# Kernel optimization log

Measured on AMD Instinct MI355X. Metric: run time of the kernel, lower is better.

Reference implementation:

```python
import jax, jax.numpy as jnp
import numpy as np

D_MODEL = 1024
N_HEADS = 16
B, T = 2, 2048


def setup_inputs() -> dict:
    key = jax.random.key(0)
    kx, kqkv, ko = jax.random.split(key, 3)
    x = jax.random.normal(kx, (B, T, D_MODEL), dtype=jnp.float32)
    # flax Linear default init (lecun_normal ~ scaled); plain scaled normal is fine for a baseline
    Wqkv = jax.random.normal(kqkv, (D_MODEL, 3 * D_MODEL), dtype=jnp.float32) / np.sqrt(D_MODEL)
    Wo = jax.random.normal(ko, (D_MODEL, D_MODEL), dtype=jnp.float32) / np.sqrt(D_MODEL)
    return {"x": x, "Wqkv": Wqkv, "Wo": Wo}


def reference(x, Wqkv, Wo):
    Bx, Tx, C = x.shape
    H = N_HEADS
    Hd = C // H
    scale = C ** (-0.5)  # NOTE: module scales by d_model**-0.5, not head_dim**-0.5
    qkv = x @ Wqkv  # [B, T, 3C]
    q, k, v = jnp.split(qkv, 3, axis=-1)
    q = q.reshape(Bx, Tx, H, Hd).transpose(0, 2, 1, 3)  # [B,H,T,Hd]
    k = k.reshape(Bx, Tx, H, Hd).transpose(0, 2, 1, 3)
    v = v.reshape(Bx, Tx, H, Hd).transpose(0, 2, 1, 3)
    attn = jnp.einsum('bhid,bhjd->bhij', q, k) * scale  # [B,H,T,T]
    mask = jnp.tril(jnp.ones((Tx, Tx), dtype=jnp.bool_))
    attn = jnp.where(mask[None, None], attn, jnp.finfo(attn.dtype).min)
    attn = jax.nn.softmax(attn.astype(jnp.float32), axis=-1).astype(attn.dtype)
    out = jnp.einsum('bhij,bhjd->bhid', attn, v)  # [B,H,T,Hd]
    out = out.transpose(0, 2, 1, 3).reshape(Bx, Tx, C)
    return out @ Wo
```

## Files before the change

### kernel.cpp

```cpp
#include <hip/hip_runtime.h>
#include <cstdint>
#include <math.h>

#define D_MODEL 1024
#define N_HEADS 16
#define HEAD_DIM 64
#define BB 2
#define TT 2048
#define QSCALE 0.04508422002778011f
#define MSTATIC 12.0f

typedef float f32x4 __attribute__((ext_vector_type(4)));
typedef __bf16 bf16x8 __attribute__((ext_vector_type(8)));

__device__ inline ushort f2bf(float f) {
    union { float f; uint32_t u; } c; c.f = f;
    uint32_t u = c.u;
    uint32_t r = (u + 0x7FFFu + ((u >> 16) & 1u)) >> 16;
    return (ushort)r;
}
__device__ inline ushort f2bf_hw(float f) {
    __bf16 h = (__bf16)f;
    return __builtin_bit_cast(ushort, h);
}

__device__ inline void load_lds16(const ushort* g, ushort* lds_uniform_base) {
    __builtin_amdgcn_global_load_lds(
        (const __attribute__((address_space(1))) uint32_t*)g,
        (__attribute__((address_space(3))) uint32_t*)lds_uniform_base, 16, 0, 0);
}

__global__ __launch_bounds__(256) void conv_x(
    const float4* __restrict__ in, ushort4* __restrict__ out, int n4)
{
    int i = blockIdx.x * 256 + threadIdx.x;
    if (i < n4) {
        float4 v = in[i];
        ushort4 u;
        u.x = f2bf(v.x); u.y = f2bf(v.y); u.z = f2bf(v.z); u.w = f2bf(v.w);
        out[i] = u;
    }
}

__global__ __launch_bounds__(256) void transpose_f32_bf16(
    const float* __restrict__ in, ushort* __restrict__ out, int R, int C)
{
    __shared__ ushort tile[32][33];
    int tx = threadIdx.x;
    int ty = threadIdx.y;
    int c0 = blockIdx.x * 32;
    int r0 = blockIdx.y * 32;
#pragma unroll
    for (int i = 0; i < 32; i += 8)
        tile[ty + i][tx] = f2bf(in[(size_t)(r0 + ty + i) * C + (c0 + tx)]);
    __syncthreads();
#pragma unroll
    for (int i = 0; i < 32; i += 8)
        out[(size_t)(c0 + ty + i) * R + (r0 + tx)] = tile[tx][ty + i];
}

__global__ __launch_bounds__(256) void transpose_v_bf16(
    const ushort* __restrict__ in, ushort* __restrict__ out)
{
    int z = blockIdx.z;
    const ushort* ip = in + (size_t)z * TT * HEAD_DIM;
    ushort* op = out + (size_t)z * TT * HEAD_DIM;
    __shared__ ushort tile[32][33];
    int tx = threadIdx.x, ty = threadIdx.y;
    int d0 = blockIdx.x * 32;
    int t0 = blockIdx.y * 32;
#pragma unroll
    for (int i = 0; i < 32; i += 8)
        tile[ty + i][tx] = ip[(size_t)(t0 + ty + i) * HEAD_DIM + d0 + tx];
    __syncthreads();
#pragma unroll
    for (int i = 0; i < 32; i += 8)
        op[(size_t)(d0 + ty + i) * TT + t0 + tx] = tile[tx][ty + i];
}

__device__ inline void gemm128_mainloop(
    const ushort* __restrict__ A, const ushort* __restrict__ BT,
    int rowBase, int colBase, ushort* Al, ushort* Bl,
    f32x4 acc[4][4], int wave, int lane)
{
    const int K = D_MODEL;
    int lr = lane & 15, quad = lane >> 4;
    int lrow = lane >> 2;
    int kq = lane & 3;
    int mq = (wave >> 1) * 64, nq = (wave & 1) * 64;

    const ushort* gA0 = A + (size_t)(rowBase + wave * 32 + lrow) * K + kq * 8;
    const ushort* gA1 = gA0 + (size_t)16 * K;
    const ushort* gB0 = BT + (size_t)(colBase + wave * 32 + lrow) * K + kq * 8;
    const ushort* gB1 = gB0 + (size_t)16 * K;
    ushort* lA0 = Al + (wave * 32) * 32;
    ushort* lA1 = Al + (wave * 32 + 16) * 32;
    ushort* lB0 = Bl + (wave * 32) * 32;
    ushort* lB1 = Bl + (wave * 32 + 16) * 32;

    for (int kt = 0; kt < K / 32; ++kt) {
        __syncthreads();
        int ko = kt * 32;
        load_lds16(gA0 + ko, lA0);
        load_lds16(gA1 + ko, lA1);
        load_lds16(gB0 + ko, lB0);
        load_lds16(gB1 + ko, lB1);
        __syncthreads();
        bf16x8 af[4], bf[4];
#pragma unroll
        for (int mi = 0; mi < 4; ++mi)
            af[mi] = *(const bf16x8*)(Al + (mq + mi * 16 + lr) * 32 + quad * 8);
#pragma unroll
        for (int ni = 0; ni < 4; ++ni)
            bf[ni] = *(const bf16x8*)(Bl + (nq + ni * 16 + lr) * 32 + quad * 8);
#pragma unroll
        for (int mi = 0; mi < 4; ++mi)
#pragma unroll
            for (int ni = 0; ni < 4; ++ni)
                acc[mi][ni] = __builtin_amdgcn_mfma_f32_16x16x32_bf16(
                    af[mi], bf[ni], acc[mi][ni], 0, 0, 0);
    }
}

__global__ __launch_bounds__(256) void gemm_qkv(
    const ushort* __restrict__ A, const ushort* __restrict__ BT,
    ushort* __restrict__ Qo, ushort* __restrict__ Ko, ushort* __restrict__ Vo)
{
    __shared__ ushort Al[128 * 32];
    __shared__ ushort Bl[128 * 32];
    int tid = threadIdx.x;
    int wave = tid >> 6, lane = tid & 63;
    int lr = lane & 15, quad = lane >> 4;
    int rowBase = blockIdx.y * 128;
    int colBase = blockIdx.x * 128;
    f32x4 acc[4][4] = {};
    gemm128_mainloop(A, BT, rowBase, colBase, Al, Bl, acc, wave, lane);

    int mq = (wave >> 1) * 64, nq = (wave & 1) * 64;
#pragma unroll
    for (int ni = 0; ni < 4; ++ni) {
        int n = colBase + nq + ni * 16 + lr;
        int s = n >> 10;
        int cc = n & 1023;
        int h = cc >> 6, d = cc & 63;
        ushort* dst = (s == 0) ? Qo : (s == 1 ? Ko : Vo);
        float scale = (s == 0) ? QSCALE : 1.0f;
#pragma unroll
        for (int mi = 0; mi < 4; ++mi) {
#pragma unroll
            for (int i = 0; i < 4; ++i) {
                int m = rowBase + mq + mi * 16 + quad * 4 + i;
                int b = m >> 11, t = m & 2047;
                int bh = b * N_HEADS + h;
                dst[((size_t)bh * TT + t) * HEAD_DIM + d] = f2bf(acc[mi][ni][i] * scale);
            }
        }
    }
}

__global__ __launch_bounds__(256) void gemm_plain(
    const ushort* __restrict__ A, const ushort* __restrict__ BT,
    float* __restrict__ O, int N)
{
    const int K = D_MODEL;
    __shared__ ushort Al[128 * 32];
    __shared__ ushort Bl[64 * 32];
    int tid = threadIdx.x;
    int wave = tid >> 6, lane = tid & 63;
    int lr = lane & 15, quad = lane >> 4;
    int lrow = lane >> 2, kq = lane & 3;
    int rowBase = blockIdx.y * 128;
    int colBase = blockIdx.x * 64;
    int mq = (wave >> 1) * 64, nq = (wave & 1) * 32;

    const ushort* gA0 = A + (size_t)(rowBase + wave * 32 + lrow) * K + kq * 8;
    const ushort* gA1 = gA0 + (size_t)16 * K;
    const ushort* gB0 = BT + (size_t)(colBase + wave * 32 + lrow) * K + kq * 8;
    const ushort* gB1 = gB0 + (size_t)16 * K;
    ushort* lA0 = Al + (wave * 32) * 32;
    ushort* lA1 = Al + (wave * 32 + 16) * 32;
    ushort* lB0 = Bl + (wave * 32) * 32;
    ushort* lB1 = Bl + (wave * 32 + 16) * 32;

    f32x4 acc[4][2] = {};
    for (int kt = 0; kt < K / 32; ++kt) {
        __syncthreads();
        int ko = kt * 32;
        load_lds16(gA0 + ko, lA0);
        load_lds16(gA1 + ko, lA1);
        if (wave < 2) {
            load_lds16(gB0 + ko, lB0);
            load_lds16(gB1 + ko, lB1);
        }
        __syncthreads();
        bf16x8 af[4], bf[2];
#pragma unroll
        for (int mi = 0; mi < 4; ++mi)
            af[mi] = *(const bf16x8*)(Al + (mq + mi * 16 + lr) * 32 + quad * 8);
#pragma unroll
        for (int ni = 0; ni < 2; ++ni)
            bf[ni] = *(const bf16x8*)(Bl + (nq + ni * 16 + lr) * 32 + quad * 8);
#pragma unroll
        for (int mi = 0; mi < 4; ++mi)
#pragma unroll
            for (int ni = 0; ni < 2; ++ni)
                acc[mi][ni] = __builtin_amdgcn_mfma_f32_16x16x32_bf16(
                    af[mi], bf[ni], acc[mi][ni], 0, 0, 0);
    }

#pragma unroll
    for (int mi = 0; mi < 4; ++mi)
#pragma unroll
        for (int ni = 0; ni < 2; ++ni) {
            int n = colBase + nq + ni * 16 + lr;
#pragma unroll
            for (int i = 0; i < 4; ++i) {
                int m = rowBase + mq + mi * 16 + quad * 4 + i;
                O[(size_t)m * N + n] = acc[mi][ni][i];
            }
        }
}

__global__ __launch_bounds__(512) void attn_flash(
    const ushort* __restrict__ Q,
    const ushort* __restrict__ K,
    const ushort* __restrict__ VT,
    ushort* __restrict__ AO)
{
    int bid = blockIdx.x;
    int bh  = bid & 31;
    int idx = bid >> 5;
    int qi  = (idx < 8) ? idx : (23 - idx);
    int tid = threadIdx.x;
    int wave = tid >> 6;
    int pair = wave & 3;
    int half = wave >> 2;
    int lane = tid & 63;
    int quad = lane >> 4, lr = lane & 15;
    int qw = qi * 128 + pair * 32;

    const ushort* Qb = Q  + (size_t)bh * TT * HEAD_DIM;
    const ushort* Kb = K  + (size_t)bh * TT * HEAD_DIM;
    const ushort* Vb = VT + (size_t)bh * HEAD_DIM * TT;

    __shared__ ushort pbuf[8][32][40];
    __shared__ float comb[4][10][64][4];
    ushort (*P)[40] = pbuf[wave];

    bf16x8 qa[2][2];
#pragma unroll
    for (int r = 0; r < 2; ++r)
#pragma unroll
        for (int s = 0; s < 2; ++s)
            qa[r][s] = *(const bf16x8*)(Qb + (size_t)(qw + r * 16 + lr) * HEAD_DIM
                                           + s * 32 + quad * 8);

    f32x4 o[2][4] = {};
    f32x4 l[2] = {};

    bf16x8 ones;
#pragma unroll
    for (int j = 0; j < 8; ++j) ones[j] = (__bf16)1.0f;

    int ktiles = (qw >> 5) + 1;
    bf16x8 kbp[2][2], vbp[4];
    if (half < ktiles) {
        int k0 = half << 5;
#pragma unroll
        for (int c = 0; c < 2; ++c)
#pragma unroll
            for (int s = 0; s < 2; ++s)
                kbp[c][s] = *(const bf16x8*)(Kb + (size_t)(k0 + c * 16 + lr) * HEAD_DIM
                                                + s * 32 + quad * 8);
#pragma unroll
        for (int d = 0; d < 4; ++d)
            vbp[d] = *(const bf16x8*)(Vb + (size_t)(d * 16 + lr) * TT + k0 + quad * 8);
    }

    for (int kt = half; kt < ktiles; kt += 2) {
        bf16x8 kb[2][2], vb[4];
#pragma unroll
        for (int c = 0; c < 2; ++c)
#pragma unroll
            for (int s = 0; s < 2; ++s) kb[c][s] = kbp[c][s];
#pragma unroll
        for (int d = 0; d < 4; ++d) vb[d] = vbp[d];

        int kn = kt + 2;
        if (kn < ktiles) {
            int k0n = kn << 5;
#pragma unroll
            for (int c = 0; c < 2; ++c)
#pragma unroll
                for (int s = 0; s < 2; ++s)
                    kbp[c][s] = *(const bf16x8*)(Kb + (size_t)(k0n + c * 16 + lr) * HEAD_DIM
                                                    + s * 32 + quad * 8);
#pragma unroll
            for (int d = 0; d < 4; ++d)
                vbp[d] = *(const bf16x8*)(Vb + (size_t)(d * 16 + lr) * TT + k0n + quad * 8);
        }

        f32x4 sc[2][2];
#pragma unroll
        for (int r = 0; r < 2; ++r)
#pragma unroll
            for (int c = 0; c < 2; ++c)
#pragma unroll
                for (int i = 0; i < 4; ++i) sc[r][c][i] = -MSTATIC;
#pragma unroll
        for (int r = 0; r < 2; ++r)
#pragma unroll
            for (int c = 0; c < 2; ++c) {
                sc[r][c] = __builtin_amdgcn_mfma_f32_16x16x32_bf16(qa[r][0], kb[c][0], sc[r][c], 0, 0, 0);
                sc[r][c] = __builtin_amdgcn_mfma_f32_16x16x32_bf16(qa[r][1], kb[c][1], sc[r][c], 0, 0, 0);
            }
        if (kt == ktiles - 1) {
#pragma unroll
            for (int r = 0; r < 2; ++r)
#pragma unroll
                for (int c = 0; c < 2; ++c)
#pragma unroll
                    for (int i = 0; i < 4; ++i)
                        if (c * 16 + lr > r * 16 + quad * 4 + i) sc[r][c][i] = -3e38f;
        }

#pragma unroll
        for (int r = 0; r < 2; ++r)
#pragma unroll
            for (int c = 0; c < 2; ++c)
#pragma unroll
                for (int i = 0; i < 4; ++i)
                    P[r * 16 + quad * 4 + i][c * 16 + lr] =
                        f2bf_hw(__builtin_amdgcn_exp2f(sc[r][c][i]));

#pragma unroll
        for (int r = 0; r < 2; ++r) {
            bf16x8 pa = *(const bf16x8*)&P[r * 16 + lr][quad * 8];
            l[r] = __builtin_amdgcn_mfma_f32_16x16x32_bf16(pa, ones, l[r], 0, 0, 0);
#pragma unroll
            for (int d = 0; d < 4; ++d)
                o[r][d] = __builtin_amdgcn_mfma_f32_16x16x32_bf16(pa, vb[d], o[r][d], 0, 0, 0);
        }
    }

    if (half == 1) {
#pragma unroll
        for (int r = 0; r < 2; ++r)
#pragma unroll
            for (int d = 0; d < 4; ++d)
                *(f32x4*)&comb[pair][r * 4 + d][lane][0] = o[r][d];
#pragma unroll
        for (int r = 0; r < 2; ++r)
            *(f32x4*)&comb[pair][8 + r][lane][0] = l[r];
    }
    __syncthreads();
    if (half == 0) {
#pragma unroll
        for (int r = 0; r < 2; ++r)
#pragma unroll
            for (int d = 0; d < 4; ++d)
                o[r][d] += *(const f32x4*)&comb[pair][r * 4 + d][lane][0];
#pragma unroll
        for (int r = 0; r < 2; ++r)
            l[r] += *(const f32x4*)&comb[pair][8 + r][lane][0];

        int b = bh >> 4, h = bh & 15;
#pragma unroll
        for (int r = 0; r < 2; ++r) {
            f32x4 rl;
#pragma unroll
            for (int i = 0; i < 4; ++i) rl[i] = 1.0f / l[r][i];
#pragma unroll
            for (int d = 0; d < 4; ++d)
#pragma unroll
                for (int i = 0; i < 4; ++i) {
                    int row = qw + r * 16 + quad * 4 + i;
                    AO[((size_t)(b * TT + row)) * D_MODEL + h * HEAD_DIM + d * 16 + lr] =
                        f2bf(o[r][d][i] * rl[i]);
                }
        }
    }
}

extern "C" void kernel_launch(void* const* d_in, const int* in_sizes, int n_in,
                              void* d_out, int out_size, void* d_ws, size_t ws_size,
                              hipStream_t stream)
{
    (void)in_sizes; (void)n_in; (void)out_size; (void)ws_size;
    const float* x    = (const float*)d_in[0];
    const float* Wqkv = (const float*)d_in[1];
    const float* Wo   = (const float*)d_in[2];
    float* out = (float*)d_out;

    char* ws = (char*)d_ws;
    size_t off = 0;
    ushort* WqkvT = (ushort*)(ws + off); off += (size_t)3 * D_MODEL * D_MODEL * 2;
    ushort* WoT   = (ushort*)(ws + off); off += (size_t)D_MODEL * D_MODEL * 2;
    ushort* xb    = (ushort*)(ws + off); off += (size_t)BB * TT * D_MODEL * 2;
    ushort* Qd    = (ushort*)(ws + off); off += (size_t)BB * D_MODEL * TT * 2;
    ushort* Kd    = (ushort*)(ws + off); off += (size_t)BB * D_MODEL * TT * 2;
    ushort* Vd    = (ushort*)(ws + off); off += (size_t)BB * D_MODEL * TT * 2;
    ushort* VTd   = (ushort*)(ws + off); off += (size_t)BB * D_MODEL * TT * 2;
    ushort* AO    = (ushort*)(ws + off); off += (size_t)BB * TT * D_MODEL * 2;

    int n4 = BB * TT * D_MODEL / 4;
    conv_x<<<dim3(n4 / 256), 256, 0, stream>>>(
        (const float4*)x, (ushort4*)xb, n4);

    transpose_f32_bf16<<<dim3(3 * D_MODEL / 32, D_MODEL / 32), dim3(32, 8), 0, stream>>>(
        Wqkv, WqkvT, D_MODEL, 3 * D_MODEL);
    transpose_f32_bf16<<<dim3(D_MODEL / 32, D_MODEL / 32), dim3(32, 8), 0, stream>>>(
        Wo, WoT, D_MODEL, D_MODEL);

    gemm_qkv<<<dim3(3 * D_MODEL / 128, BB * TT / 128), 256, 0, stream>>>(
        xb, WqkvT, Qd, Kd, Vd);

    transpose_v_bf16<<<dim3(HEAD_DIM / 32, TT / 32, BB * N_HEADS), dim3(32, 8), 0, stream>>>(
        Vd, VTd);

    attn_flash<<<dim3(512), 512, 0, stream>>>(Qd, Kd, VTd, AO);

    gemm_plain<<<dim3(D_MODEL / 64, BB * TT / 128), 256, 0, stream>>>(
        AO, WoT, out, D_MODEL);
}
```

Before: 213.7 us.

## Share K/V tiles across waves via LDS and drop split-KV wave pairs

Flash attention now uses 4 waves per block instead of 8. Each wave owns 32 query rows and walks the full key range itself, so the two-half split and the LDS combine step are gone. Each K/V tile is loaded once into double-buffered LDS and read by all four waves, replacing per-wave global loads of the same tiles. The cost is two block barriers per tile with no explicit prefetch overlap, half the threads per block, and early waves sitting idle on tiles past their causal limit.

```diff
diff --git a/kernel.cpp b/kernel.cpp
--- a/kernel.cpp
+++ b/kernel.cpp
@@ -221,7 +221,7 @@
         }
 }
 
-__global__ __launch_bounds__(512) void attn_flash(
+__global__ __launch_bounds__(256) void attn_flash(
     const ushort* __restrict__ Q,
     const ushort* __restrict__ K,
     const ushort* __restrict__ VT,
@@ -232,20 +232,24 @@
     int idx = bid >> 5;
     int qi  = (idx < 8) ? idx : (23 - idx);
     int tid = threadIdx.x;
-    int wave = tid >> 6;
-    int pair = wave & 3;
-    int half = wave >> 2;
-    int lane = tid & 63;
+    int wave = tid >> 6, lane = tid & 63;
     int quad = lane >> 4, lr = lane & 15;
-    int qw = qi * 128 + pair * 32;
+    int qb = qi * 128;
+    int qw = qb + wave * 32;
 
     const ushort* Qb = Q  + (size_t)bh * TT * HEAD_DIM;
     const ushort* Kb = K  + (size_t)bh * TT * HEAD_DIM;
     const ushort* Vb = VT + (size_t)bh * HEAD_DIM * TT;
 
-    __shared__ ushort pbuf[8][32][40];
-    __shared__ float comb[4][10][64][4];
+    __shared__ ushort Kl[2][32 * 64];
+    __shared__ ushort Vl[2][64 * 32];
+    __shared__ ushort pbuf[4][32][40];
     ushort (*P)[40] = pbuf[wave];
+
+    int krow = lane >> 3, kchunk = lane & 7;
+    int vrow = lane >> 2, vchunk = lane & 3;
+    const ushort* gK = Kb + (size_t)(wave * 8 + krow) * HEAD_DIM + kchunk * 8;
+    const ushort* gV = Vb + (size_t)(wave * 16 + vrow) * TT + vchunk * 8;
 
     bf16x8 qa[2][2];
 #pragma unroll
@@ -262,123 +266,85 @@
 #pragma unroll
     for (int j = 0; j < 8; ++j) ones[j] = (__bf16)1.0f;
 
-    int ktiles = (qw >> 5) + 1;
-    bf16x8 kbp[2][2], vbp[4];
-    if (half < ktiles) {
-        int k0 = half << 5;
-#pragma unroll
-        for (int c = 0; c < 2; ++c)
-#pragma unroll
-            for (int s = 0; s < 2; ++s)
-                kbp[c][s] = *(const bf16x8*)(Kb + (size_t)(k0 + c * 16 + lr) * HEAD_DIM
-                                                + s * 32 + quad * 8);
+    int myktiles = (qw >> 5) + 1;
+    int blocktiles = (qb >> 5) + 4;
+
+    for (int kt = 0; kt < blocktiles; ++kt) {
+        int buf = kt & 1;
+        __syncthreads();
+        load_lds16(gK + (size_t)(kt * 32) * HEAD_DIM, &Kl[buf][wave * 512]);
+        load_lds16(gV + kt * 32,                      &Vl[buf][wave * 512]);
+        __syncthreads();
+
+        if (kt < myktiles) {
+            bf16x8 kb[2][2], vb[4];
+#pragma unroll
+            for (int c = 0; c < 2; ++c)
+#pragma unroll
+                for (int s = 0; s < 2; ++s)
+                    kb[c][s] = *(const bf16x8*)&Kl[buf][(c * 16 + lr) * 64 + s * 32 + quad * 8];
+#pragma unroll
+            for (int d = 0; d < 4; ++d)
+                vb[d] = *(const bf16x8*)&Vl[buf][(d * 16 + lr) * 32 + quad * 8];
+
+            f32x4 sc[2][2];
+#pragma unroll
+            for (int r = 0; r < 2; ++r)
+#pragma unroll
+                for (int c = 0; c < 2; ++c)
+#pragma unroll
+                    for (int i = 0; i < 4; ++i) sc[r][c][i] = -MSTATIC;
+#pragma unroll
+            for (int r = 0; r < 2; ++r)
+#pragma unroll
+                for (int c = 0; c < 2; ++c) {
+                    sc[r][c] = __builtin_amdgcn_mfma_f32_16x16x32_bf16(qa[r][0], kb[c][0], sc[r][c], 0, 0, 0);
+                    sc[r][c] = __builtin_amdgcn_mfma_f32_16x16x32_bf16(qa[r][1], kb[c][1], sc[r][c], 0, 0, 0);
+                }
+            if (kt == myktiles - 1) {
+#pragma unroll
+                for (int r = 0; r < 2; ++r)
+#pragma unroll
+                    for (int c = 0; c < 2; ++c)
+#pragma unroll
+                        for (int i = 0; i < 4; ++i)
+                            if (c * 16 + lr > r * 16 + quad * 4 + i) sc[r][c][i] = -3e38f;
+            }
+
+#pragma unroll
+            for (int r = 0; r < 2; ++r)
+#pragma unroll
+                for (int c = 0; c < 2; ++c)
+#pragma unroll
+                    for (int i = 0; i < 4; ++i)
+                        P[r * 16 + quad * 4 + i][c * 16 + lr] =
+                            f2bf_hw(__builtin_amdgcn_exp2f(sc[r][c][i]));
+
+#pragma unroll
+            for (int r = 0; r < 2; ++r) {
+                bf16x8 pa = *(const bf16x8*)&P[r * 16 + lr][quad * 8];
+                l[r] = __builtin_amdgcn_mfma_f32_16x16x32_bf16(pa, ones, l[r], 0, 0, 0);
+#pragma unroll
+                for (int d = 0; d < 4; ++d)
+                    o[r][d] = __builtin_amdgcn_mfma_f32_16x16x32_bf16(pa, vb[d], o[r][d], 0, 0, 0);
+            }
+        }
+    }
+
+    int b = bh >> 4, h = bh & 15;
+#pragma unroll
+    for (int r = 0; r < 2; ++r) {
+        f32x4 rl;
+#pragma unroll
+        for (int i = 0; i < 4; ++i) rl[i] = 1.0f / l[r][i];
 #pragma unroll
         for (int d = 0; d < 4; ++d)
-            vbp[d] = *(const bf16x8*)(Vb + (size_t)(d * 16 + lr) * TT + k0 + quad * 8);
-    }
-
-    for (int kt = half; kt < ktiles; kt += 2) {
-        bf16x8 kb[2][2], vb[4];
-#pragma unroll
-        for (int c = 0; c < 2; ++c)
-#pragma unroll
-            for (int s = 0; s < 2; ++s) kb[c][s] = kbp[c][s];
-#pragma unroll
-        for (int d = 0; d < 4; ++d) vb[d] = vbp[d];
-
-        int kn = kt + 2;
-        if (kn < ktiles) {
-            int k0n = kn << 5;
-#pragma unroll
-            for (int c = 0; c < 2; ++c)
-#pragma unroll
-                for (int s = 0; s < 2; ++s)
-                    kbp[c][s] = *(const bf16x8*)(Kb + (size_t)(k0n + c * 16 + lr) * HEAD_DIM
-                                                    + s * 32 + quad * 8);
-#pragma unroll
-            for (int d = 0; d < 4; ++d)
-                vbp[d] = *(const bf16x8*)(Vb + (size_t)(d * 16 + lr) * TT + k0n + quad * 8);
-        }
-
-        f32x4 sc[2][2];
-#pragma unroll
-        for (int r = 0; r < 2; ++r)
-#pragma unroll
-            for (int c = 0; c < 2; ++c)
-#pragma unroll
-                for (int i = 0; i < 4; ++i) sc[r][c][i] = -MSTATIC;
-#pragma unroll
-        for (int r = 0; r < 2; ++r)
-#pragma unroll
-            for (int c = 0; c < 2; ++c) {
-                sc[r][c] = __builtin_amdgcn_mfma_f32_16x16x32_bf16(qa[r][0], kb[c][0], sc[r][c], 0, 0, 0);
-                sc[r][c] = __builtin_amdgcn_mfma_f32_16x16x32_bf16(qa[r][1], kb[c][1], sc[r][c], 0, 0, 0);
-            }
-        if (kt == ktiles - 1) {
-#pragma unroll
-            for (int r = 0; r < 2; ++r)
-#pragma unroll
-                for (int c = 0; c < 2; ++c)
-#pragma unroll
-                    for (int i = 0; i < 4; ++i)
-                        if (c * 16 + lr > r * 16 + quad * 4 + i) sc[r][c][i] = -3e38f;
-        }
-
-#pragma unroll
-        for (int r = 0; r < 2; ++r)
-#pragma unroll
-            for (int c = 0; c < 2; ++c)
-#pragma unroll
-                for (int i = 0; i < 4; ++i)
-                    P[r * 16 + quad * 4 + i][c * 16 + lr] =
-                        f2bf_hw(__builtin_amdgcn_exp2f(sc[r][c][i]));
-
-#pragma unroll
-        for (int r = 0; r < 2; ++r) {
-            bf16x8 pa = *(const bf16x8*)&P[r * 16 + lr][quad * 8];
-            l[r] = __builtin_amdgcn_mfma_f32_16x16x32_bf16(pa, ones, l[r], 0, 0, 0);
-#pragma unroll
-            for (int d = 0; d < 4; ++d)
-                o[r][d] = __builtin_amdgcn_mfma_f32_16x16x32_bf16(pa, vb[d], o[r][d], 0, 0, 0);
-        }
-    }
-
-    if (half == 1) {
-#pragma unroll
-        for (int r = 0; r < 2; ++r)
-#pragma unroll
-            for (int d = 0; d < 4; ++d)
-                *(f32x4*)&comb[pair][r * 4 + d][lane][0] = o[r][d];
-#pragma unroll
-        for (int r = 0; r < 2; ++r)
-            *(f32x4*)&comb[pair][8 + r][lane][0] = l[r];
-    }
-    __syncthreads();
-    if (half == 0) {
-#pragma unroll
-        for (int r = 0; r < 2; ++r)
-#pragma unroll
-            for (int d = 0; d < 4; ++d)
-                o[r][d] += *(const f32x4*)&comb[pair][r * 4 + d][lane][0];
-#pragma unroll
-        for (int r = 0; r < 2; ++r)
-            l[r] += *(const f32x4*)&comb[pair][8 + r][lane][0];
-
-        int b = bh >> 4, h = bh & 15;
-#pragma unroll
-        for (int r = 0; r < 2; ++r) {
-            f32x4 rl;
-#pragma unroll
-            for (int i = 0; i < 4; ++i) rl[i] = 1.0f / l[r][i];
-#pragma unroll
-            for (int d = 0; d < 4; ++d)
-#pragma unroll
-                for (int i = 0; i < 4; ++i) {
-                    int row = qw + r * 16 + quad * 4 + i;
-                    AO[((size_t)(b * TT + row)) * D_MODEL + h * HEAD_DIM + d * 16 + lr] =
-                        f2bf(o[r][d][i] * rl[i]);
-                }
-        }
+#pragma unroll
+            for (int i = 0; i < 4; ++i) {
+                int row = qw + r * 16 + quad * 4 + i;
+                AO[((size_t)(b * TT + row)) * D_MODEL + h * HEAD_DIM + d * 16 + lr] =
+                    f2bf(o[r][d][i] * rl[i]);
+            }
     }
 }
 
@@ -418,7 +384,7 @@
     transpose_v_bf16<<<dim3(HEAD_DIM / 32, TT / 32, BB * N_HEADS), dim3(32, 8), 0, stream>>>(
         Vd, VTd);
 
-    attn_flash<<<dim3(512), 512, 0, stream>>>(Qd, Kd, VTd, AO);
+    attn_flash<<<dim3(512), 256, 0, stream>>>(Qd, Kd, VTd, AO);
 
     gemm_plain<<<dim3(D_MODEL / 64, BB * TT / 128), 256, 0, stream>>>(
         AO, WoT, out, D_MODEL);
```

New measurement: 214.5 us. No clear change (+0.4%).
